# Performance work log

Hardware: AMD Instinct MI355X
Metric: run time of the kernel (lower is better)

## Reference

```python
import jax, jax.numpy as jnp
import numpy as np

HEADS, DIM_HEAD = 8, 64
EPS = 1e-5  # torch InstanceNorm1d default


def instance_norm(t):
    # torch InstanceNorm1d(dim_head) applied to (b*h, n, d) normalizes over the
    # last dim d for each (b, h, n); affine=False, biased variance.
    mu = jnp.mean(t, axis=-1, keepdims=True)
    var = jnp.mean((t - mu) ** 2, axis=-1, keepdims=True)
    return (t - mu) * jax.lax.rsqrt(var + EPS)


def setup_inputs() -> dict:
    key = jax.random.key(0)
    k1, k2, k3, k4 = jax.random.split(key, 4)
    B, N, D = 8, 8192, 256
    inner = HEADS * DIM_HEAD  # 512
    x = jax.random.normal(k1, (B, N, D), jnp.float32)
    w_qkv = jax.random.normal(k2, (3 * inner, D), jnp.float32) / np.sqrt(D).astype(np.float32)
    w_out = jax.random.normal(k3, (D, inner), jnp.float32) / np.sqrt(inner).astype(np.float32)
    b_out = 0.01 * jax.random.normal(k4, (D,), jnp.float32)
    return {"x": x, "w_qkv": w_qkv, "w_out": w_out, "b_out": b_out}


def reference(x, w_qkv, w_out, b_out):
    B, N, _ = x.shape
    H, Dh = HEADS, DIM_HEAD
    # fused qkv projection: [B,N,3*H*Dh]
    qkv = jnp.einsum('bnd,ed->bne', x, w_qkv)
    q, k, v = jnp.split(qkv, 3, axis=-1)

    def to_heads(t):
        return t.reshape(B, N, H, Dh).transpose(0, 2, 1, 3)  # b h n d

    q, k, v = to_heads(q), to_heads(k), to_heads(v)
    # galerkin: instance-norm K and V
    k = instance_norm(k)
    v = instance_norm(v)
    # linear (non-softmax) attention: (K^T V) then Q @ (K^T V), scaled by 1/N
    dots = jnp.einsum('bhnd,bhne->bhde', k, v)            # [B,H,Dh,Dh]
    out = jnp.einsum('bhnd,bhde->bhne', q, dots) / N      # [B,H,N,Dh]
    out = out.transpose(0, 2, 1, 3).reshape(B, N, H * Dh)
    return jnp.einsum('bne,de->bnd', out, w_out) + b_out
```

## Files before the change

### kernel.cpp

```cpp
#include <hip/hip_runtime.h>
#include <hip/hip_bf16.h>
#include <stdint.h>

typedef __attribute__((ext_vector_type(8))) __bf16 bf16x8;
typedef __attribute__((ext_vector_type(8))) unsigned short ushort8_t;
typedef __attribute__((ext_vector_type(4))) unsigned short ushort4_t;
typedef __attribute__((ext_vector_type(4))) float f32x4;

#define MFMA16(a, b, c) __builtin_amdgcn_mfma_f32_16x16x32_bf16((a), (b), (c), 0, 0, 0)

static __device__ __forceinline__ unsigned short f2bf(float f) {
  union { float f; unsigned u; } v; v.f = f;
  unsigned r = v.u + 0x7fffu + ((v.u >> 16) & 1u);
  return (unsigned short)(r >> 16);
}
static __device__ __forceinline__ float bf2f(unsigned short u) {
  union { unsigned u; float f; } v; v.u = ((unsigned)u) << 16; return v.f;
}

static __device__ __forceinline__ void gld_lds16(const void* g, void* l) {
  __builtin_amdgcn_global_load_lds((const __attribute__((address_space(1))) void*)g,
                                   (__attribute__((address_space(3))) void*)l, 16, 0, 0);
}

__global__ __launch_bounds__(256) void k_convx(const float* __restrict__ x,
                                               unsigned short* __restrict__ xb) {
  size_t i = ((size_t)blockIdx.x * 256 + threadIdx.x) * 4;
  float4 v = *(const float4*)(x + i);
  ushort4_t o = { f2bf(v.x), f2bf(v.y), f2bf(v.z), f2bf(v.w) };
  *(ushort4_t*)(xb + i) = o;
}

__global__ void k_convw(const float* __restrict__ w, unsigned short* __restrict__ wb) {
  int i = (blockIdx.x * 256 + threadIdx.x) * 4;
  float4 v = *(const float4*)(w + i);
  ushort4_t o = { f2bf(v.x), f2bf(v.y), f2bf(v.z), f2bf(v.w) };
  *(ushort4_t*)(wb + i) = o;
}

__global__ void k_convo(const float* __restrict__ w, unsigned short* __restrict__ wb) {
  int i = (blockIdx.x * 256 + threadIdx.x) * 4;
  float4 v = *(const float4*)(w + i);
  ushort4_t o = { f2bf(v.x), f2bf(v.y), f2bf(v.z), f2bf(v.w) };
  *(ushort4_t*)(wb + i) = o;
}

__global__ __launch_bounds__(512) void k_gemm1(const unsigned short* __restrict__ xb,
                                               const unsigned short* __restrict__ wqb,
                                               unsigned short* __restrict__ kvb) {
  __shared__ unsigned short As[2][16384];
  __shared__ unsigned short Bs[2][16384];
  const int t = threadIdx.x;
  const int w = t >> 6, lane = t & 63, lr = lane & 15, lg = lane >> 4;
  const int wr = w >> 2, wc = w & 3;

  const int id = blockIdx.x;
  const int nid = (id & 7) * 128 + (id >> 3);
  const int nt = nid & 3, mt = nid >> 2;
  const long m0 = (long)mt * 256;
  const int e0 = 512 + nt * 256;

  const int srl = lane >> 3, sc = lane & 7;

#pragma unroll
  for (int i = 0; i < 2; ++i) {
    const int r = (w * 2 + i) * 8 + srl;
    const int cs = (sc ^ (r & 7)) << 3;
    gld_lds16(xb + (size_t)(m0 + r) * 256 + cs,          &As[0][(w * 2 + i) * 512]);
    gld_lds16(xb + (size_t)(m0 + 128 + r) * 256 + cs,    &As[0][8192 + (w * 2 + i) * 512]);
    gld_lds16(wqb + (size_t)(e0 + r) * 256 + cs,         &Bs[0][(w * 2 + i) * 512]);
    gld_lds16(wqb + (size_t)(e0 + 128 + r) * 256 + cs,   &Bs[0][8192 + (w * 2 + i) * 512]);
  }
  __syncthreads();

  f32x4 acc[8][4];
#pragma unroll
  for (int i = 0; i < 8; ++i)
#pragma unroll
    for (int j = 0; j < 4; ++j) acc[i][j] = f32x4{0.f, 0.f, 0.f, 0.f};

  bf16x8 a[4][2], b[2][2][2];

  for (int kt = 0; kt < 4; ++kt) {
    const int cur = kt & 1, nxt = cur ^ 1;
    const int kn0 = (kt + 1) * 64;
    const bool st = kt < 3;

#pragma unroll
    for (int mb = 0; mb < 4; ++mb) {
      const int R = wr * 128 + mb * 16 + lr;
#pragma unroll
      for (int kh = 0; kh < 2; ++kh)
        a[mb][kh] = *(const bf16x8*)&As[cur][R * 64 + ((((kh << 2) + lg) ^ (R & 7)) << 3)];
    }
#pragma unroll
    for (int nb = 0; nb < 2; ++nb) {
      const int E = wc * 64 + nb * 16 + lr;
#pragma unroll
      for (int kh = 0; kh < 2; ++kh)
        b[0][nb][kh] = *(const bf16x8*)&Bs[cur][E * 64 + ((((kh << 2) + lg) ^ (E & 7)) << 3)];
    }
    if (st) {
#pragma unroll
      for (int i = 0; i < 2; ++i) {
        const int r = (w * 2 + i) * 8 + srl;
        gld_lds16(xb + (size_t)(m0 + r) * 256 + kn0 + ((sc ^ (r & 7)) << 3),
                  &As[nxt][(w * 2 + i) * 512]);
      }
    }
    __builtin_amdgcn_s_barrier();
    __builtin_amdgcn_s_setprio(1);
#pragma unroll
    for (int mb = 0; mb < 4; ++mb)
#pragma unroll
      for (int nb = 0; nb < 2; ++nb)
#pragma unroll
        for (int kh = 0; kh < 2; ++kh)
          acc[mb][nb] = MFMA16(a[mb][kh], b[0][nb][kh], acc[mb][nb]);
    __builtin_amdgcn_s_setprio(0);
    __builtin_amdgcn_s_barrier();

#pragma unroll
    for (int nb = 0; nb < 2; ++nb) {
      const int E = wc * 64 + 32 + nb * 16 + lr;
#pragma unroll
      for (int kh = 0; kh < 2; ++kh)
        b[1][nb][kh] = *(const bf16x8*)&Bs[cur][E * 64 + ((((kh << 2) + lg) ^ (E & 7)) << 3)];
    }
    if (st) {
#pragma unroll
      for (int i = 0; i < 2; ++i) {
        const int r = (w * 2 + i) * 8 + srl;
        gld_lds16(xb + (size_t)(m0 + 128 + r) * 256 + kn0 + ((sc ^ (r & 7)) << 3),
                  &As[nxt][8192 + (w * 2 + i) * 512]);
      }
    }
    __builtin_amdgcn_s_barrier();
    __builtin_amdgcn_s_setprio(1);
#pragma unroll
    for (int mb = 0; mb < 4; ++mb)
#pragma unroll
      for (int nb = 0; nb < 2; ++nb)
#pragma unroll
        for (int kh = 0; kh < 2; ++kh)
          acc[mb][2 + nb] = MFMA16(a[mb][kh], b[1][nb][kh], acc[mb][2 + nb]);
    __builtin_amdgcn_s_setprio(0);
    __builtin_amdgcn_s_barrier();

#pragma unroll
    for (int mb = 0; mb < 4; ++mb) {
      const int R = wr * 128 + 64 + mb * 16 + lr;
#pragma unroll
      for (int kh = 0; kh < 2; ++kh)
        a[mb][kh] = *(const bf16x8*)&As[cur][R * 64 + ((((kh << 2) + lg) ^ (R & 7)) << 3)];
    }
    if (st) {
#pragma unroll
      for (int i = 0; i < 2; ++i) {
        const int r = (w * 2 + i) * 8 + srl;
        gld_lds16(wqb + (size_t)(e0 + r) * 256 + kn0 + ((sc ^ (r & 7)) << 3),
                  &Bs[nxt][(w * 2 + i) * 512]);
      }
    }
    __builtin_amdgcn_s_barrier();
    __builtin_amdgcn_s_setprio(1);
#pragma unroll
    for (int mb = 0; mb < 4; ++mb)
#pragma unroll
      for (int nb = 0; nb < 2; ++nb)
#pragma unroll
        for (int kh = 0; kh < 2; ++kh)
          acc[4 + mb][nb] = MFMA16(a[mb][kh], b[0][nb][kh], acc[4 + mb][nb]);
    __builtin_amdgcn_s_setprio(0);
    __builtin_amdgcn_s_barrier();

    if (st) {
#pragma unroll
      for (int i = 0; i < 2; ++i) {
        const int r = (w * 2 + i) * 8 + srl;
        gld_lds16(wqb + (size_t)(e0 + 128 + r) * 256 + kn0 + ((sc ^ (r & 7)) << 3),
                  &Bs[nxt][8192 + (w * 2 + i) * 512]);
      }
    }
    __builtin_amdgcn_s_barrier();
    __builtin_amdgcn_s_setprio(1);
#pragma unroll
    for (int mb = 0; mb < 4; ++mb)
#pragma unroll
      for (int nb = 0; nb < 2; ++nb)
#pragma unroll
        for (int kh = 0; kh < 2; ++kh)
          acc[4 + mb][2 + nb] = MFMA16(a[mb][kh], b[1][nb][kh], acc[4 + mb][2 + nb]);
    __builtin_amdgcn_s_setprio(0);
    __syncthreads();
  }

#pragma unroll
  for (int i = 0; i < 8; ++i) {
    const long row0 = m0 + wr * 128 + (i >> 2) * 64 + (i & 3) * 16 + lg * 4;
#pragma unroll
    for (int j = 0; j < 4; ++j) {
      const int col = nt * 256 + wc * 64 + (j >> 1) * 32 + (j & 1) * 16 + lr;
#pragma unroll
      for (int rg = 0; rg < 4; ++rg)
        kvb[(size_t)(row0 + rg) * 1024 + col] = f2bf(acc[i][j][rg]);
    }
  }
}

__global__ __launch_bounds__(256) void k_dots(const unsigned short* __restrict__ kvb,
                                              float* __restrict__ partials) {
  __shared__ unsigned short ktl[2][64 * 72];
  __shared__ unsigned short vtl[2][64 * 72];
  const int bh = blockIdx.x, ch = blockIdx.y;
  const int b = bh >> 3, h = bh & 7;
  const int t = threadIdx.x;
  const int w = t >> 6, lane = t & 63, lr = lane & 15, lg = lane >> 4;
  const unsigned short* kbase = kvb + ((size_t)b * 8192) * 1024 + h * 64;
  const int r = t >> 2, q4 = t & 3;
  const int n00 = ch * 1024;
  f32x4 acc[4];
#pragma unroll
  for (int eb = 0; eb < 4; ++eb) acc[eb] = f32x4{0.f, 0.f, 0.f, 0.f};

  ushort8_t rA[4], rB[4];
  {
    const unsigned short* krow = kbase + (size_t)(n00 + r) * 1024 + q4 * 16;
    rA[0] = *(const ushort8_t*)krow;
    rA[1] = *(const ushort8_t*)(krow + 8);
    rA[2] = *(const ushort8_t*)(krow + 512);
    rA[3] = *(const ushort8_t*)(krow + 520);
  }

#define DOTS_BODY(RC, RN, NT)                                                     \
  {                                                                               \
    float kf[16], vf[16];                                                         \
    _Pragma("unroll") for (int i = 0; i < 8; ++i) {                               \
      kf[i] = bf2f(RC[0][i]); kf[i + 8] = bf2f(RC[1][i]);                         \
      vf[i] = bf2f(RC[2][i]); vf[i + 8] = bf2f(RC[3][i]);                         \
    }                                                                             \
    float ksum = 0, ksq = 0, vsum = 0, vsq = 0;                                   \
    _Pragma("unroll") for (int i = 0; i < 16; ++i) {                              \
      ksum += kf[i]; ksq += kf[i] * kf[i];                                        \
      vsum += vf[i]; vsq += vf[i] * vf[i];                                        \
    }                                                                             \
    ksum += __shfl_xor(ksum, 1); ksq += __shfl_xor(ksq, 1);                       \
    vsum += __shfl_xor(vsum, 1); vsq += __shfl_xor(vsq, 1);                       \
    ksum += __shfl_xor(ksum, 2); ksq += __shfl_xor(ksq, 2);                       \
    vsum += __shfl_xor(vsum, 2); vsq += __shfl_xor(vsq, 2);                       \
    const float kmean = ksum * (1.f / 64.f);                                      \
    const float krs = rsqrtf(ksq * (1.f / 64.f) - kmean * kmean + 1e-5f);         \
    const float vmean = vsum * (1.f / 64.f);                                      \
    const float vrs = rsqrtf(vsq * (1.f / 64.f) - vmean * vmean + 1e-5f);         \
    const int cu = (NT) & 1;                                                      \
    _Pragma("unroll") for (int i = 0; i < 16; ++i) {                              \
      int d = q4 * 16 + i;                                                        \
      ktl[cu][d * 72 + r] = f2bf((kf[i] - kmean) * krs);                          \
      vtl[cu][d * 72 + r] = f2bf((vf[i] - vmean) * vrs);                          \
    }                                                                             \
    if ((NT) + 1 < 16) {                                                          \
      const unsigned short* krow2 =                                               \
          kbase + (size_t)(n00 + ((NT) + 1) * 64 + r) * 1024 + q4 * 16;           \
      RN[0] = *(const ushort8_t*)krow2;                                           \
      RN[1] = *(const ushort8_t*)(krow2 + 8);                                     \
      RN[2] = *(const ushort8_t*)(krow2 + 512);                                   \
      RN[3] = *(const ushort8_t*)(krow2 + 520);                                   \
    }                                                                             \
    __syncthreads();                                                              \
    _Pragma("unroll") for (int ns = 0; ns < 64; ns += 32) {                       \
      bf16x8 af = *(const bf16x8*)&ktl[cu][(16 * w + lr) * 72 + ns + lg * 8];     \
      _Pragma("unroll") for (int eb = 0; eb < 4; ++eb) {                          \
        bf16x8 bv = *(const bf16x8*)&vtl[cu][(16 * eb + lr) * 72 + ns + lg * 8];  \
        acc[eb] = MFMA16(af, bv, acc[eb]);                                        \
      }                                                                           \
    }                                                                             \
  }

  for (int nt = 0; nt < 16; nt += 2) {
    DOTS_BODY(rA, rB, nt);
    DOTS_BODY(rB, rA, nt + 1);
  }
#undef DOTS_BODY

  float* pb = partials + ((size_t)ch * 64 + bh) * 4096;
#pragma unroll
  for (int eb = 0; eb < 4; ++eb)
#pragma unroll
    for (int rg = 0; rg < 4; ++rg) {
      int d = 16 * w + lg * 4 + rg;
      int e = 16 * eb + lr;
      pb[d * 64 + e] = acc[eb][rg];
    }
}

__global__ __launch_bounds__(256) void k_mmat(const float* __restrict__ partials,
                                              const float* __restrict__ wqkv,
                                              unsigned short* __restrict__ tmpT) {
  __shared__ float dl[4096];
  __shared__ float wqls[64 * 256];
  const int bh = blockIdx.x, b = bh >> 3, h = bh & 7;
  const int t = threadIdx.x;
#pragma unroll
  for (int i = 0; i < 4; ++i) {
    int off = t * 16 + i * 4;
    f32x4 s = {0.f, 0.f, 0.f, 0.f};
    for (int c = 0; c < 8; ++c) {
      f32x4 p = *(const f32x4*)(partials + ((size_t)c * 64 + bh) * 4096 + off);
      s += p;
    }
    *(f32x4*)&dl[off] = s;
  }
#pragma unroll
  for (int i = 0; i < 16; ++i) {
    int idx4 = i * 256 + t;
    int d = idx4 >> 6, c4 = idx4 & 63;
    *(f32x4*)&wqls[d * 256 + c4 * 4] =
        *(const f32x4*)(wqkv + (size_t)(h * 64 + d) * 256 + c4 * 4);
  }
  __syncthreads();
  const int k = t;
  const float scale = 1.0f / 8192.0f;
  float res[64];
  for (int e = 0; e < 64; ++e) {
    float s = 0.f;
#pragma unroll
    for (int d = 0; d < 64; ++d) s += dl[d * 64 + e] * wqls[d * 256 + k];
    res[e] = s * scale;
  }
  unsigned short* dst = tmpT + (size_t)b * 131072 + (size_t)k * 512 + h * 64;
#pragma unroll
  for (int e8 = 0; e8 < 8; ++e8) {
    ushort8_t o;
#pragma unroll
    for (int j = 0; j < 8; ++j) o[j] = f2bf(res[e8 * 8 + j]);
    *(ushort8_t*)(dst + e8 * 8) = o;
  }
}

__global__ __launch_bounds__(256) void k_pmat(const unsigned short* __restrict__ woutb,
                                              const unsigned short* __restrict__ tmpT,
                                              unsigned short* __restrict__ pswz) {
  const int bid = blockIdx.x;
  const int b = bid >> 2, oq = (bid >> 1) & 1, kq = bid & 1;
  const int t = threadIdx.x, w = t >> 6, lane = t & 63, lr = lane & 15, lg = lane >> 4;
  const int wr = w >> 1, wc = w & 1;
  const int ob = oq * 128 + wr * 64, kb = kq * 128 + wc * 64;
  const unsigned short* tb = tmpT + (size_t)b * 131072;

  f32x4 acc[4][4];
#pragma unroll
  for (int mb = 0; mb < 4; ++mb)
#pragma unroll
    for (int nb = 0; nb < 4; ++nb) acc[mb][nb] = f32x4{0.f, 0.f, 0.f, 0.f};

  for (int ks = 0; ks < 16; ++ks) {
    bf16x8 a[4], bb[4];
#pragma unroll
    for (int mb = 0; mb < 4; ++mb)
      a[mb] = *(const bf16x8*)(woutb + (size_t)(ob + mb * 16 + lr) * 512 + ks * 32 + lg * 8);
#pragma unroll
    for (int nb = 0; nb < 4; ++nb)
      bb[nb] = *(const bf16x8*)(tb + (size_t)(kb + nb * 16 + lr) * 512 + ks * 32 + lg * 8);
#pragma unroll
    for (int mb = 0; mb < 4; ++mb)
#pragma unroll
      for (int nb = 0; nb < 4; ++nb) acc[mb][nb] = MFMA16(a[mb], bb[nb], acc[mb][nb]);
  }

  unsigned short* pb = pswz + (size_t)b * 65536;
#pragma unroll
  for (int mb = 0; mb < 4; ++mb)
#pragma unroll
    for (int nb = 0; nb < 4; ++nb)
#pragma unroll
      for (int rg = 0; rg < 4; ++rg) {
        int o = ob + mb * 16 + lg * 4 + rg;
        int k = kb + nb * 16 + lr;
        pb[(((k >> 5) * 16 + (o >> 4)) * 64 + (o & 15) + ((k >> 3) & 3) * 16) * 8 + (k & 7)] =
            f2bf(acc[mb][nb][rg]);
      }
}

__global__ __launch_bounds__(512) void k_gemm2(const unsigned short* __restrict__ xb,
                                               const unsigned short* __restrict__ pswz,
                                               const float* __restrict__ bout,
                                               float* __restrict__ out) {
  __shared__ unsigned short As[2][128 * 64];
  const int b = blockIdx.x >> 6, mt = blockIdx.x & 63;
  const long m0 = (long)mt * 128;
  const int t = threadIdx.x, w = t >> 6, lane = t & 63, lr = lane & 15, lg = lane >> 4;
  const int wr = w >> 2, wc = w & 3;
  const unsigned short* qb = xb + ((size_t)b * 8192 + m0) * 256;
  const unsigned short* Mb = pswz + (size_t)b * 65536;
  const int srl = lane >> 3, sc = lane & 7;

#pragma unroll
  for (int i = 0; i < 2; ++i) {
    const int row = (i * 8 + w) * 8 + srl;
    gld_lds16(qb + (size_t)row * 256 + ((sc ^ (row & 7)) << 3),
              &As[0][(i * 8 + w) * 512]);
  }
  __syncthreads();

  f32x4 acc[4][4];
#pragma unroll
  for (int mb = 0; mb < 4; ++mb)
#pragma unroll
    for (int nb = 0; nb < 4; ++nb) acc[mb][nb] = f32x4{0.f, 0.f, 0.f, 0.f};

  for (int ks = 0; ks < 4; ++ks) {
    const int cur = ks & 1, nxt = cur ^ 1;
    if (ks < 3) {
      const int k0 = (ks + 1) * 64;
#pragma unroll
      for (int i = 0; i < 2; ++i) {
        const int row = (i * 8 + w) * 8 + srl;
        gld_lds16(qb + (size_t)row * 256 + k0 + ((sc ^ (row & 7)) << 3),
                  &As[nxt][(i * 8 + w) * 512]);
      }
    }
    bf16x8 a[4][2], bfr[2][4];
#pragma unroll
    for (int mb = 0; mb < 4; ++mb) {
      const int R = wr * 64 + mb * 16 + lr;
#pragma unroll
      for (int kh = 0; kh < 2; ++kh)
        a[mb][kh] = *(const bf16x8*)&As[cur][R * 64 + ((((kh << 2) + lg) ^ (R & 7)) << 3)];
    }
#pragma unroll
    for (int kh = 0; kh < 2; ++kh)
#pragma unroll
      for (int nb = 0; nb < 4; ++nb)
        bfr[kh][nb] = *(const bf16x8*)(Mb + ((((size_t)ks * 2 + kh) * 16 + wc * 4 + nb) * 64 + lane) * 8);
#pragma unroll
    for (int mb = 0; mb < 4; ++mb)
#pragma unroll
      for (int nb = 0; nb < 4; ++nb)
#pragma unroll
        for (int kh = 0; kh < 2; ++kh)
          acc[mb][nb] = MFMA16(a[mb][kh], bfr[kh][nb], acc[mb][nb]);
    __syncthreads();
  }

  float bo[4];
#pragma unroll
  for (int nb = 0; nb < 4; ++nb) bo[nb] = bout[wc * 64 + nb * 16 + lr];
  float* ob = out + ((size_t)b * 8192 + m0) * 256;
#pragma unroll
  for (int mb = 0; mb < 4; ++mb)
#pragma unroll
    for (int nb = 0; nb < 4; ++nb)
#pragma unroll
      for (int rg = 0; rg < 4; ++rg) {
        int row = wr * 64 + mb * 16 + lg * 4 + rg;
        int c = wc * 64 + nb * 16 + lr;
        ob[(size_t)row * 256 + c] = acc[mb][nb][rg] + bo[nb];
      }
}

extern "C" void kernel_launch(void* const* d_in, const int* in_sizes, int n_in,
                              void* d_out, int out_size, void* d_ws, size_t ws_size,
                              hipStream_t stream) {
  const float* x    = (const float*)d_in[0];
  const float* wqkv = (const float*)d_in[1];
  const float* wout = (const float*)d_in[2];
  const float* bout = (const float*)d_in[3];
  float* out = (float*)d_out;

  char* ws = (char*)d_ws;
  unsigned short* kvb = (unsigned short*)ws;
  size_t off = (size_t)65536 * 1024 * 2;
  unsigned short* xb = (unsigned short*)(ws + off);
  off += (size_t)65536 * 256 * 2;
  unsigned short* wqb = (unsigned short*)(ws + off);
  off += (size_t)1536 * 256 * 2;
  unsigned short* woutb = (unsigned short*)(ws + off);
  off += (size_t)256 * 512 * 2;
  float* partials = (float*)(ws + off);
  off += (size_t)8 * 64 * 4096 * 4;
  unsigned short* tmpT = (unsigned short*)(ws + off);
  off += (size_t)8 * 131072 * 2;
  unsigned short* pswz = (unsigned short*)(ws + off);
  off += (size_t)8 * 65536 * 2;

  k_convx<<<16384, 256, 0, stream>>>(x, xb);
  k_convw<<<384, 256, 0, stream>>>(wqkv, wqb);
  k_convo<<<128, 256, 0, stream>>>(wout, woutb);
  k_gemm1<<<1024, 512, 0, stream>>>(xb, wqb, kvb);
  dim3 gd(64, 8);
  k_dots<<<gd, 256, 0, stream>>>(kvb, partials);
  k_mmat<<<64, 256, 0, stream>>>(partials, wqkv, tmpT);
  k_pmat<<<32, 256, 0, stream>>>(woutb, tmpT, pswz);
  k_gemm2<<<512, 512, 0, stream>>>(xb, pswz, bout, out);
}
```

Measured before the change: 183.9 us.

## Fuse K/V projection, instance norm and K^T V into one kernel

The K/V projection GEMM, per-row instance normalization and per-head K^T V partial products now run in a single kernel. Each block computes a 256-row by (K,V for one head) tile, normalizes it in registers, transposes it into LDS and accumulates a partial 64x64 dots matrix. This removes the write and re-read of the 128MB bf16 K/V intermediate, at the cost of more partials (32 per batch-head) to reduce and a simpler pipeline without the interleaved barrier/setprio scheduling. The x tile is now reloaded once per head, so x is read eight times from global/L2.

After: 169.8 us. 7.7% less time.

```diff
diff --git a/kernel.cpp b/kernel.cpp
--- a/kernel.cpp
+++ b/kernel.cpp
@@ -45,251 +45,123 @@
   *(ushort4_t*)(wb + i) = o;
 }
 
-__global__ __launch_bounds__(512) void k_gemm1(const unsigned short* __restrict__ xb,
+__global__ __launch_bounds__(512) void k_fused(const unsigned short* __restrict__ xb,
                                                const unsigned short* __restrict__ wqb,
-                                               unsigned short* __restrict__ kvb) {
-  __shared__ unsigned short As[2][16384];
-  __shared__ unsigned short Bs[2][16384];
+                                               float* __restrict__ partials) {
+  __shared__ __align__(16) char smem[98304];
+  unsigned short* As = (unsigned short*)smem;
+  unsigned short* Bs = (unsigned short*)(smem + 65536);
+  unsigned short* kt = (unsigned short*)smem;
+  unsigned short* vt = (unsigned short*)(smem + 36864);
+
   const int t = threadIdx.x;
   const int w = t >> 6, lane = t & 63, lr = lane & 15, lg = lane >> 4;
-  const int wr = w >> 2, wc = w & 3;
+  const int wr = w >> 1, wc = w & 1;
 
   const int id = blockIdx.x;
-  const int nid = (id & 7) * 128 + (id >> 3);
-  const int nt = nid & 3, mt = nid >> 2;
+  const int nid = (id & 7) * 256 + (id >> 3);
+  const int mt = nid >> 3, h = nid & 7;
   const long m0 = (long)mt * 256;
-  const int e0 = 512 + nt * 256;
-
-  const int srl = lane >> 3, sc = lane & 7;
-
-#pragma unroll
-  for (int i = 0; i < 2; ++i) {
-    const int r = (w * 2 + i) * 8 + srl;
-    const int cs = (sc ^ (r & 7)) << 3;
-    gld_lds16(xb + (size_t)(m0 + r) * 256 + cs,          &As[0][(w * 2 + i) * 512]);
-    gld_lds16(xb + (size_t)(m0 + 128 + r) * 256 + cs,    &As[0][8192 + (w * 2 + i) * 512]);
-    gld_lds16(wqb + (size_t)(e0 + r) * 256 + cs,         &Bs[0][(w * 2 + i) * 512]);
-    gld_lds16(wqb + (size_t)(e0 + 128 + r) * 256 + cs,   &Bs[0][8192 + (w * 2 + i) * 512]);
-  }
+
+  const unsigned short* bk = wqb + (size_t)(512 + h * 64) * 256;
+  const unsigned short* bv = wqb + (size_t)(1024 + h * 64) * 256;
+
+  const int srl = t >> 3, sc = t & 7;
+  const int swz = (sc ^ (srl & 7)) << 3;
+
+#pragma unroll
+  for (int i = 0; i < 4; ++i)
+    gld_lds16(xb + (size_t)(m0 + i * 64 + srl) * 256 + swz, &As[i * 4096 + t * 8]);
+  gld_lds16(bk + (size_t)srl * 256 + swz, &Bs[t * 8]);
+  gld_lds16(bv + (size_t)srl * 256 + swz, &Bs[4096 + t * 8]);
   __syncthreads();
 
-  f32x4 acc[8][4];
-#pragma unroll
-  for (int i = 0; i < 8; ++i)
-#pragma unroll
-    for (int j = 0; j < 4; ++j) acc[i][j] = f32x4{0.f, 0.f, 0.f, 0.f};
-
-  bf16x8 a[4][2], b[2][2][2];
-
-  for (int kt = 0; kt < 4; ++kt) {
-    const int cur = kt & 1, nxt = cur ^ 1;
-    const int kn0 = (kt + 1) * 64;
-    const bool st = kt < 3;
-
+  f32x4 acc[4][4];
+#pragma unroll
+  for (int mb = 0; mb < 4; ++mb)
+#pragma unroll
+    for (int nb = 0; nb < 4; ++nb) acc[mb][nb] = f32x4{0.f, 0.f, 0.f, 0.f};
+
+  for (int ks = 0; ks < 4; ++ks) {
+    const int cur = ks & 1, nxt = cur ^ 1;
+    if (ks < 3) {
+      const int k0 = (ks + 1) * 64;
+#pragma unroll
+      for (int i = 0; i < 4; ++i)
+        gld_lds16(xb + (size_t)(m0 + i * 64 + srl) * 256 + k0 + swz,
+                  &As[nxt * 16384 + i * 4096 + t * 8]);
+      gld_lds16(bk + (size_t)srl * 256 + k0 + swz, &Bs[nxt * 8192 + t * 8]);
+      gld_lds16(bv + (size_t)srl * 256 + k0 + swz, &Bs[nxt * 8192 + 4096 + t * 8]);
+    }
+    bf16x8 a[4][2], b[4][2];
 #pragma unroll
     for (int mb = 0; mb < 4; ++mb) {
-      const int R = wr * 128 + mb * 16 + lr;
+      const int R = wr * 64 + mb * 16 + lr;
 #pragma unroll
       for (int kh = 0; kh < 2; ++kh)
-        a[mb][kh] = *(const bf16x8*)&As[cur][R * 64 + ((((kh << 2) + lg) ^ (R & 7)) << 3)];
-    }
-#pragma unroll
-    for (int nb = 0; nb < 2; ++nb) {
+        a[mb][kh] = *(const bf16x8*)&As[cur * 16384 + R * 64 + ((((kh << 2) + lg) ^ (R & 7)) << 3)];
+    }
+#pragma unroll
+    for (int nb = 0; nb < 4; ++nb) {
       const int E = wc * 64 + nb * 16 + lr;
 #pragma unroll
       for (int kh = 0; kh < 2; ++kh)
-        b[0][nb][kh] = *(const bf16x8*)&Bs[cur][E * 64 + ((((kh << 2) + lg) ^ (E & 7)) << 3)];
-    }
-    if (st) {
-#pragma unroll
-      for (int i = 0; i < 2; ++i) {
-        const int r = (w * 2 + i) * 8 + srl;
-        gld_lds16(xb + (size_t)(m0 + r) * 256 + kn0 + ((sc ^ (r & 7)) << 3),
-                  &As[nxt][(w * 2 + i) * 512]);
+        b[nb][kh] = *(const bf16x8*)&Bs[cur * 8192 + E * 64 + ((((kh << 2) + lg) ^ (E & 7)) << 3)];
+    }
+#pragma unroll
+    for (int mb = 0; mb < 4; ++mb)
+#pragma unroll
+      for (int nb = 0; nb < 4; ++nb)
+#pragma unroll
+        for (int kh = 0; kh < 2; ++kh)
+          acc[mb][nb] = MFMA16(a[mb][kh], b[nb][kh], acc[mb][nb]);
+    __syncthreads();
+  }
+
+  unsigned short* dst = (wc == 0 ? kt : vt) + wr * 4608;
+#pragma unroll
+  for (int mb = 0; mb < 4; ++mb) {
+#pragma unroll
+    for (int rg = 0; rg < 4; ++rg) {
+      float s1 = acc[mb][0][rg] + acc[mb][1][rg] + acc[mb][2][rg] + acc[mb][3][rg];
+      float s2 = acc[mb][0][rg] * acc[mb][0][rg] + acc[mb][1][rg] * acc[mb][1][rg] +
+                 acc[mb][2][rg] * acc[mb][2][rg] + acc[mb][3][rg] * acc[mb][3][rg];
+      s1 += __shfl_xor(s1, 1); s2 += __shfl_xor(s2, 1);
+      s1 += __shfl_xor(s1, 2); s2 += __shfl_xor(s2, 2);
+      s1 += __shfl_xor(s1, 4); s2 += __shfl_xor(s2, 4);
+      s1 += __shfl_xor(s1, 8); s2 += __shfl_xor(s2, 8);
+      const float mean = s1 * (1.f / 64.f);
+      const float rs = rsqrtf(s2 * (1.f / 64.f) - mean * mean + 1e-5f);
+      const int nn = mb * 16 + lg * 4 + rg;
+#pragma unroll
+      for (int nb = 0; nb < 4; ++nb)
+        dst[(nb * 16 + lr) * 72 + nn] = f2bf((acc[mb][nb][rg] - mean) * rs);
+    }
+  }
+  __syncthreads();
+
+  const int dblk = w >> 1, ep = w & 1;
+  f32x4 acc2[2] = {f32x4{0.f, 0.f, 0.f, 0.f}, f32x4{0.f, 0.f, 0.f, 0.f}};
+#pragma unroll
+  for (int cn = 0; cn < 4; ++cn) {
+#pragma unroll
+    for (int ns = 0; ns < 64; ns += 32) {
+      bf16x8 af = *(const bf16x8*)&kt[cn * 4608 + (dblk * 16 + lr) * 72 + ns + lg * 8];
+#pragma unroll
+      for (int e = 0; e < 2; ++e) {
+        bf16x8 bvf = *(const bf16x8*)&vt[cn * 4608 + ((ep * 2 + e) * 16 + lr) * 72 + ns + lg * 8];
+        acc2[e] = MFMA16(af, bvf, acc2[e]);
       }
     }
-    __builtin_amdgcn_s_barrier();
-    __builtin_amdgcn_s_setprio(1);
-#pragma unroll
-    for (int mb = 0; mb < 4; ++mb)
-#pragma unroll
-      for (int nb = 0; nb < 2; ++nb)
-#pragma unroll
-        for (int kh = 0; kh < 2; ++kh)
-          acc[mb][nb] = MFMA16(a[mb][kh], b[0][nb][kh], acc[mb][nb]);
-    __builtin_amdgcn_s_setprio(0);
-    __builtin_amdgcn_s_barrier();
-
-#pragma unroll
-    for (int nb = 0; nb < 2; ++nb) {
-      const int E = wc * 64 + 32 + nb * 16 + lr;
-#pragma unroll
-      for (int kh = 0; kh < 2; ++kh)
-        b[1][nb][kh] = *(const bf16x8*)&Bs[cur][E * 64 + ((((kh << 2) + lg) ^ (E & 7)) << 3)];
-    }
-    if (st) {
-#pragma unroll
-      for (int i = 0; i < 2; ++i) {
-        const int r = (w * 2 + i) * 8 + srl;
-        gld_lds16(xb + (size_t)(m0 + 128 + r) * 256 + kn0 + ((sc ^ (r & 7)) << 3),
-                  &As[nxt][8192 + (w * 2 + i) * 512]);
-      }
-    }
-    __builtin_amdgcn_s_barrier();
-    __builtin_amdgcn_s_setprio(1);
-#pragma unroll
-    for (int mb = 0; mb < 4; ++mb)
-#pragma unroll
-      for (int nb = 0; nb < 2; ++nb)
-#pragma unroll
-        for (int kh = 0; kh < 2; ++kh)
-          acc[mb][2 + nb] = MFMA16(a[mb][kh], b[1][nb][kh], acc[mb][2 + nb]);
-    __builtin_amdgcn_s_setprio(0);
-    __builtin_amdgcn_s_barrier();
-
-#pragma unroll
-    for (int mb = 0; mb < 4; ++mb) {
-      const int R = wr * 128 + 64 + mb * 16 + lr;
-#pragma unroll
-      for (int kh = 0; kh < 2; ++kh)
-        a[mb][kh] = *(const bf16x8*)&As[cur][R * 64 + ((((kh << 2) + lg) ^ (R & 7)) << 3)];
-    }
-    if (st) {
-#pragma unroll
-      for (int i = 0; i < 2; ++i) {
-        const int r = (w * 2 + i) * 8 + srl;
-        gld_lds16(wqb + (size_t)(e0 + r) * 256 + kn0 + ((sc ^ (r & 7)) << 3),
-                  &Bs[nxt][(w * 2 + i) * 512]);
-      }
-    }
-    __builtin_amdgcn_s_barrier();
-    __builtin_amdgcn_s_setprio(1);
-#pragma unroll
-    for (int mb = 0; mb < 4; ++mb)
-#pragma unroll
-      for (int nb = 0; nb < 2; ++nb)
-#pragma unroll
-        for (int kh = 0; kh < 2; ++kh)
-          acc[4 + mb][nb] = MFMA16(a[mb][kh], b[0][nb][kh], acc[4 + mb][nb]);
-    __builtin_amdgcn_s_setprio(0);
-    __builtin_amdgcn_s_barrier();
-
-    if (st) {
-#pragma unroll
-      for (int i = 0; i < 2; ++i) {
-        const int r = (w * 2 + i) * 8 + srl;
-        gld_lds16(wqb + (size_t)(e0 + 128 + r) * 256 + kn0 + ((sc ^ (r & 7)) << 3),
-                  &Bs[nxt][8192 + (w * 2 + i) * 512]);
-      }
-    }
-    __builtin_amdgcn_s_barrier();
-    __builtin_amdgcn_s_setprio(1);
-#pragma unroll
-    for (int mb = 0; mb < 4; ++mb)
-#pragma unroll
-      for (int nb = 0; nb < 2; ++nb)
-#pragma unroll
-        for (int kh = 0; kh < 2; ++kh)
-          acc[4 + mb][2 + nb] = MFMA16(a[mb][kh], b[1][nb][kh], acc[4 + mb][2 + nb]);
-    __builtin_amdgcn_s_setprio(0);
-    __syncthreads();
-  }
-
-#pragma unroll
-  for (int i = 0; i < 8; ++i) {
-    const long row0 = m0 + wr * 128 + (i >> 2) * 64 + (i & 3) * 16 + lg * 4;
-#pragma unroll
-    for (int j = 0; j < 4; ++j) {
-      const int col = nt * 256 + wc * 64 + (j >> 1) * 32 + (j & 1) * 16 + lr;
-#pragma unroll
-      for (int rg = 0; rg < 4; ++rg)
-        kvb[(size_t)(row0 + rg) * 1024 + col] = f2bf(acc[i][j][rg]);
-    }
-  }
-}
-
-__global__ __launch_bounds__(256) void k_dots(const unsigned short* __restrict__ kvb,
-                                              float* __restrict__ partials) {
-  __shared__ unsigned short ktl[2][64 * 72];
-  __shared__ unsigned short vtl[2][64 * 72];
-  const int bh = blockIdx.x, ch = blockIdx.y;
-  const int b = bh >> 3, h = bh & 7;
-  const int t = threadIdx.x;
-  const int w = t >> 6, lane = t & 63, lr = lane & 15, lg = lane >> 4;
-  const unsigned short* kbase = kvb + ((size_t)b * 8192) * 1024 + h * 64;
-  const int r = t >> 2, q4 = t & 3;
-  const int n00 = ch * 1024;
-  f32x4 acc[4];
-#pragma unroll
-  for (int eb = 0; eb < 4; ++eb) acc[eb] = f32x4{0.f, 0.f, 0.f, 0.f};
-
-  ushort8_t rA[4], rB[4];
-  {
-    const unsigned short* krow = kbase + (size_t)(n00 + r) * 1024 + q4 * 16;
-    rA[0] = *(const ushort8_t*)krow;
-    rA[1] = *(const ushort8_t*)(krow + 8);
-    rA[2] = *(const ushort8_t*)(krow + 512);
-    rA[3] = *(const ushort8_t*)(krow + 520);
-  }
-
-#define DOTS_BODY(RC, RN, NT)                                                     \
-  {                                                                               \
-    float kf[16], vf[16];                                                         \
-    _Pragma("unroll") for (int i = 0; i < 8; ++i) {                               \
-      kf[i] = bf2f(RC[0][i]); kf[i + 8] = bf2f(RC[1][i]);                         \
-      vf[i] = bf2f(RC[2][i]); vf[i + 8] = bf2f(RC[3][i]);                         \
-    }                                                                             \
-    float ksum = 0, ksq = 0, vsum = 0, vsq = 0;                                   \
-    _Pragma("unroll") for (int i = 0; i < 16; ++i) {                              \
-      ksum += kf[i]; ksq += kf[i] * kf[i];                                        \
-      vsum += vf[i]; vsq += vf[i] * vf[i];                                        \
-    }                                                                             \
-    ksum += __shfl_xor(ksum, 1); ksq += __shfl_xor(ksq, 1);                       \
-    vsum += __shfl_xor(vsum, 1); vsq += __shfl_xor(vsq, 1);                       \
-    ksum += __shfl_xor(ksum, 2); ksq += __shfl_xor(ksq, 2);                       \
-    vsum += __shfl_xor(vsum, 2); vsq += __shfl_xor(vsq, 2);                       \
-    const float kmean = ksum * (1.f / 64.f);                                      \
-    const float krs = rsqrtf(ksq * (1.f / 64.f) - kmean * kmean + 1e-5f);         \
-    const float vmean = vsum * (1.f / 64.f);                                      \
-    const float vrs = rsqrtf(vsq * (1.f / 64.f) - vmean * vmean + 1e-5f);         \
-    const int cu = (NT) & 1;                                                      \
-    _Pragma("unroll") for (int i = 0; i < 16; ++i) {                              \
-      int d = q4 * 16 + i;                                                        \
-      ktl[cu][d * 72 + r] = f2bf((kf[i] - kmean) * krs);                          \
-      vtl[cu][d * 72 + r] = f2bf((vf[i] - vmean) * vrs);                          \
-    }                                                                             \
-    if ((NT) + 1 < 16) {                                                          \
-      const unsigned short* krow2 =                                               \
-          kbase + (size_t)(n00 + ((NT) + 1) * 64 + r) * 1024 + q4 * 16;           \
-      RN[0] = *(const ushort8_t*)krow2;                                           \
-      RN[1] = *(const ushort8_t*)(krow2 + 8);                                     \
-      RN[2] = *(const ushort8_t*)(krow2 + 512);                                   \
-      RN[3] = *(const ushort8_t*)(krow2 + 520);                                   \
-    }                                                                             \
-    __syncthreads();                                                              \
-    _Pragma("unroll") for (int ns = 0; ns < 64; ns += 32) {                       \
-      bf16x8 af = *(const bf16x8*)&ktl[cu][(16 * w + lr) * 72 + ns + lg * 8];     \
-      _Pragma("unroll") for (int eb = 0; eb < 4; ++eb) {                          \
-        bf16x8 bv = *(const bf16x8*)&vtl[cu][(16 * eb + lr) * 72 + ns + lg * 8];  \
-        acc[eb] = MFMA16(af, bv, acc[eb]);                                        \
-      }                                                                           \
-    }                                                                             \
-  }
-
-  for (int nt = 0; nt < 16; nt += 2) {
-    DOTS_BODY(rA, rB, nt);
-    DOTS_BODY(rB, rA, nt + 1);
-  }
-#undef DOTS_BODY
-
-  float* pb = partials + ((size_t)ch * 64 + bh) * 4096;
-#pragma unroll
-  for (int eb = 0; eb < 4; ++eb)
+  }
+  float* pb = partials + ((size_t)mt * 8 + h) * 4096;
+#pragma unroll
+  for (int e = 0; e < 2; ++e)
 #pragma unroll
     for (int rg = 0; rg < 4; ++rg) {
-      int d = 16 * w + lg * 4 + rg;
-      int e = 16 * eb + lr;
-      pb[d * 64 + e] = acc[eb][rg];
+      int d = dblk * 16 + lg * 4 + rg;
+      int eo = (ep * 2 + e) * 16 + lr;
+      pb[d * 64 + eo] = acc2[e][rg];
     }
 }
 
@@ -304,8 +176,8 @@
   for (int i = 0; i < 4; ++i) {
     int off = t * 16 + i * 4;
     f32x4 s = {0.f, 0.f, 0.f, 0.f};
-    for (int c = 0; c < 8; ++c) {
-      f32x4 p = *(const f32x4*)(partials + ((size_t)c * 64 + bh) * 4096 + off);
+    for (int c = 0; c < 32; ++c) {
+      f32x4 p = *(const f32x4*)(partials + ((size_t)(b * 32 + c) * 8 + h) * 4096 + off);
       s += p;
     }
     *(f32x4*)&dl[off] = s;
@@ -327,13 +199,13 @@
     for (int d = 0; d < 64; ++d) s += dl[d * 64 + e] * wqls[d * 256 + k];
     res[e] = s * scale;
   }
-  unsigned short* dst = tmpT + (size_t)b * 131072 + (size_t)k * 512 + h * 64;
+  unsigned short* dstp = tmpT + (size_t)b * 131072 + (size_t)k * 512 + h * 64;
 #pragma unroll
   for (int e8 = 0; e8 < 8; ++e8) {
     ushort8_t o;
 #pragma unroll
     for (int j = 0; j < 8; ++j) o[j] = f2bf(res[e8 * 8 + j]);
-    *(ushort8_t*)(dst + e8 * 8) = o;
+    *(ushort8_t*)(dstp + e8 * 8) = o;
   }
 }
 
@@ -468,16 +340,14 @@
   float* out = (float*)d_out;
 
   char* ws = (char*)d_ws;
-  unsigned short* kvb = (unsigned short*)ws;
-  size_t off = (size_t)65536 * 1024 * 2;
-  unsigned short* xb = (unsigned short*)(ws + off);
-  off += (size_t)65536 * 256 * 2;
+  unsigned short* xb = (unsigned short*)ws;
+  size_t off = (size_t)65536 * 256 * 2;
   unsigned short* wqb = (unsigned short*)(ws + off);
   off += (size_t)1536 * 256 * 2;
   unsigned short* woutb = (unsigned short*)(ws + off);
   off += (size_t)256 * 512 * 2;
   float* partials = (float*)(ws + off);
-  off += (size_t)8 * 64 * 4096 * 4;
+  off += (size_t)2048 * 4096 * 4;
   unsigned short* tmpT = (unsigned short*)(ws + off);
   off += (size_t)8 * 131072 * 2;
   unsigned short* pswz = (unsigned short*)(ws + off);
@@ -486,9 +356,7 @@
   k_convx<<<16384, 256, 0, stream>>>(x, xb);
   k_convw<<<384, 256, 0, stream>>>(wqkv, wqb);
   k_convo<<<128, 256, 0, stream>>>(wout, woutb);
-  k_gemm1<<<1024, 512, 0, stream>>>(xb, wqb, kvb);
-  dim3 gd(64, 8);
-  k_dots<<<gd, 256, 0, stream>>>(kvb, partials);
+  k_fused<<<2048, 512, 0, stream>>>(xb, wqb, partials);
   k_mmat<<<64, 256, 0, stream>>>(partials, wqkv, tmpT);
   k_pmat<<<32, 256, 0, stream>>>(woutb, tmpT, pswz);
   k_gemm2<<<512, 512, 0, stream>>>(xb, pswz, bout, out);
```
